# Kernel tuning notes

Measured on AMD Instinct MI355X. Metric: run time of the kernel, lower is better.

Reference implementation:

```python
import jax, jax.numpy as jnp
import numpy as np

B, S, D = 2, 2048, 768
H = 12
DK = D // H  # 64; dim_q = dim_k = dim_v
DFF = 3072
EPS = 1e-5


def layer_norm(x, w, b):
    mu = jnp.mean(x, axis=-1, keepdims=True)
    var = jnp.var(x, axis=-1, keepdims=True)
    return (x - mu) * jax.lax.rsqrt(var + EPS) * w + b


def setup_inputs() -> dict:
    key = jax.random.key(0)
    ks = jax.random.split(key, 12)
    s = 0.02
    return {
        "src": jax.random.normal(ks[0], (B, S, D), dtype=jnp.float32),
        # per-head projections stacked over heads: [H, D, DK]
        "Wq": jax.random.normal(ks[1], (H, D, DK), dtype=jnp.float32) * s,
        "bq": jnp.zeros((H, DK), dtype=jnp.float32),
        "Wk": jax.random.normal(ks[2], (H, D, DK), dtype=jnp.float32) * s,
        "bk": jnp.zeros((H, DK), dtype=jnp.float32),
        "Wv": jax.random.normal(ks[3], (H, D, DK), dtype=jnp.float32) * s,
        "bv": jnp.zeros((H, DK), dtype=jnp.float32),
        # output projection: [H*DK, D]
        "Wo": jax.random.normal(ks[4], (H * DK, D), dtype=jnp.float32) * s,
        "bo": jnp.zeros((D,), dtype=jnp.float32),
        "ln1_w": jnp.ones((D,), dtype=jnp.float32),
        "ln1_b": jnp.zeros((D,), dtype=jnp.float32),
        "W1": jax.random.normal(ks[5], (D, DFF), dtype=jnp.float32) * s,
        "b1": jnp.zeros((DFF,), dtype=jnp.float32),
        "W2": jax.random.normal(ks[6], (DFF, D), dtype=jnp.float32) * s,
        "b2": jnp.zeros((D,), dtype=jnp.float32),
        "ln2_w": jnp.ones((D,), dtype=jnp.float32),
        "ln2_b": jnp.zeros((D,), dtype=jnp.float32),
    }


def reference(src, Wq, bq, Wk, bk, Wv, bv, Wo, bo, ln1_w, ln1_b,
              W1, b1, W2, b2, ln2_w, ln2_b):
    # per-head q/k/v projections, batched over heads via einsum
    q = jnp.einsum('bsd,hdk->bhsk', src, Wq) + bq[None, :, None, :]
    k = jnp.einsum('bsd,hdk->bhsk', src, Wk) + bk[None, :, None, :]
    v = jnp.einsum('bsd,hdk->bhsk', src, Wv) + bv[None, :, None, :]
    scale = jnp.asarray(DK, src.dtype) ** 0.5
    scores = jnp.einsum('bhsk,bhtk->bhst', q, k) / scale  # [B,H,S,S]
    attn = jax.nn.softmax(scores, axis=-1)
    ctx = jnp.einsum('bhst,bhtk->bhsk', attn, v)
    # concat heads along feature dim (matches torch.cat over head outputs)
    ctx = ctx.transpose(0, 2, 1, 3).reshape(src.shape[0], src.shape[1], H * DK)
    attn_out = ctx @ Wo + bo
    x = layer_norm(src + attn_out, ln1_w, ln1_b)
    ff = jax.nn.relu(x @ W1 + b1) @ W2 + b2
    return layer_norm(x + ff, ln2_w, ln2_b)
```

## Files before the change

### kernel.cpp

```cpp
#include <hip/hip_runtime.h>
#include <hip/hip_bf16.h>

#define S_LEN 2048
#define DMODEL 768
#define NHEAD 12
#define DKH 64
#define DFF_K 3072
#define MROWS 4096
#define KSPLIT 2
#define KHALF (S_LEN / KSPLIT)

typedef __attribute__((ext_vector_type(8))) short bf16x8;
typedef __attribute__((ext_vector_type(8))) unsigned short us8;
typedef __attribute__((ext_vector_type(4))) float f32x4;

__device__ __forceinline__ float bfu2f(unsigned short u) {
  return __uint_as_float(((unsigned int)u) << 16);
}
__device__ __forceinline__ unsigned short f2bfu(float f) {
  __hip_bfloat16 h = __float2bfloat16(f);
  return *reinterpret_cast<unsigned short*>(&h);
}

__device__ __forceinline__ void async16(const unsigned short* g, unsigned short* l) {
  __builtin_amdgcn_global_load_lds(
      (const __attribute__((address_space(1))) unsigned int*)g,
      (__attribute__((address_space(3))) unsigned int*)l, 16, 0, 0);
}

__global__ __launch_bounds__(256) void convert_kernel(
    const float* __restrict__ in, unsigned short* __restrict__ out, int n4)
{
  const int i = blockIdx.x * 256 + threadIdx.x;
  if (i < n4) {
    float4 v = *(const float4*)(in + (size_t)i * 4);
    ushort4 o;
    o.x = f2bfu(v.x); o.y = f2bfu(v.y); o.z = f2bfu(v.z); o.w = f2bfu(v.w);
    *(ushort4*)(out + (size_t)i * 4) = o;
  }
}

__device__ __forceinline__ void transpose_conv_body(
    const float* in, unsigned short* out, int R, int Ctot, int head,
    int bx, int by, int tid)
{
  __shared__ float t[64][68];
  const int r0 = bx * 64;
  const int c0 = by * 64;
  const float* ib;
  int ld;
  if (head) { ib = in + (size_t)by * R * 64; ld = 64; }
  else      { ib = in + c0;                  ld = Ctot; }
  const int lr = tid >> 4;
  const int lc = (tid & 15) << 2;

#pragma unroll
  for (int rr = 0; rr < 4; ++rr) {
    const int row = rr * 16 + lr;
    float4 v = *(const float4*)(ib + (size_t)(r0 + row) * ld + lc);
    t[row][lc + 0] = v.x; t[row][lc + 1] = v.y;
    t[row][lc + 2] = v.z; t[row][lc + 3] = v.w;
  }
  __syncthreads();
#pragma unroll
  for (int rr = 0; rr < 4; ++rr) {
    const int oc = rr * 16 + lr;
    ushort4 o;
    o.x = f2bfu(t[lc + 0][oc]); o.y = f2bfu(t[lc + 1][oc]);
    o.z = f2bfu(t[lc + 2][oc]); o.w = f2bfu(t[lc + 3][oc]);
    *(ushort4*)(out + (size_t)(c0 + oc) * R + r0 + lc) = o;
  }
}

__global__ __launch_bounds__(256) void transpose_conv_kernel(
    const float* __restrict__ in, unsigned short* __restrict__ out,
    int R, int Ctot, int head)
{
  transpose_conv_body(in, out, R, Ctot, head, blockIdx.x, blockIdx.y, threadIdx.x);
}

__global__ __launch_bounds__(256) void transpose_conv4_kernel(
    const float* __restrict__ i0, const float* __restrict__ i1,
    const float* __restrict__ i2, const float* __restrict__ i3,
    unsigned short* __restrict__ o0, unsigned short* __restrict__ o1,
    unsigned short* __restrict__ o2, unsigned short* __restrict__ o3)
{
  const int z = blockIdx.z;
  const float* in = (z == 0) ? i0 : (z == 1) ? i1 : (z == 2) ? i2 : i3;
  unsigned short* out = (z == 0) ? o0 : (z == 1) ? o1 : (z == 2) ? o2 : o3;
  transpose_conv_body(in, out, DMODEL, DMODEL, (z < 3) ? 1 : 0,
                      blockIdx.x, blockIdx.y, threadIdx.x);
}

template<int BN>
__device__ __forceinline__ void stage_tile(
    const unsigned short* __restrict__ Ab,
    const unsigned short* __restrict__ Bb,
    unsigned short* As, unsigned short* Bs,
    int wid, int lane, int K, int kofs)
{
  const int r = lane >> 3;
  const int s = lane & 7;
#pragma unroll
  for (int p = 0; p < 4; ++p) {
    const int row = wid * 32 + p * 8 + r;
    async16(Ab + (size_t)row * K + kofs + ((s ^ (row & 7)) << 3),
            As + (size_t)(wid * 32 + p * 8) * 64);
  }
#pragma unroll
  for (int p = 0; p < BN / 32; ++p) {
    const int row = wid * (BN / 4) + p * 8 + r;
    async16(Bb + (size_t)row * K + kofs + ((s ^ (row & 7)) << 3),
            Bs + (size_t)(wid * (BN / 4) + p * 8) * 64);
  }
}

template<int BN>
__global__ __launch_bounds__(256) void mfma_gemm_kernel(
    const unsigned short* __restrict__ A,
    const unsigned short* __restrict__ BT,
    const float* __restrict__ bias,
    unsigned short* __restrict__ C,
    int K, int N, int relu, int klen, size_t out_stride)
{
  constexpr int WN = (BN == 128) ? 64 : 32;
  constexpr int NJ = WN / 16;
  __shared__ unsigned short As[2][128][64];
  __shared__ unsigned short Bs[2][BN][64];

  const int tid  = threadIdx.x;
  const int wid  = tid >> 6;
  const int lane = tid & 63;
  const int ml   = lane & 15;
  const int quad = lane >> 4;
  const int wm   = (wid & 1) * 64;
  const int wn   = (wid >> 1) * WN;
  const int row0 = blockIdx.x * 128;
  const int col0 = blockIdx.y * BN;
  const int zed  = blockIdx.z;
  const int kb0  = zed * klen;
  const int nsteps = klen >> 6;
  const int fsw = (ml & 7) << 4;

  const unsigned short* Ab = A  + (size_t)row0 * K + kb0;
  const unsigned short* Bb = BT + (size_t)col0 * K + kb0;

  f32x4 acc[4][NJ];
#pragma unroll
  for (int i = 0; i < 4; ++i)
#pragma unroll
    for (int j = 0; j < NJ; ++j)
#pragma unroll
      for (int r = 0; r < 4; ++r) acc[i][j][r] = 0.f;

  stage_tile<BN>(Ab, Bb, &As[0][0][0], &Bs[0][0][0], wid, lane, K, 0);
  __syncthreads();

  for (int st = 0; st < nsteps; ++st) {
    const int cur = st & 1;
    if (st + 1 < nsteps)
      stage_tile<BN>(Ab, Bb, &As[cur ^ 1][0][0], &Bs[cur ^ 1][0][0],
                     wid, lane, K, (st + 1) << 6);

    const char* Ac = (const char*)&As[cur][0][0];
    const char* Bc = (const char*)&Bs[cur][0][0];
#pragma unroll
    for (int h = 0; h < 2; ++h) {
      bf16x8 af[4], bfr[NJ];
#pragma unroll
      for (int i = 0; i < 4; ++i) {
        const int ar = wm + i * 16 + ml;
        af[i] = *(const bf16x8*)(Ac + ar * 128 + (((h << 6) + (quad << 4)) ^ fsw));
      }
#pragma unroll
      for (int j = 0; j < NJ; ++j) {
        const int br = wn + j * 16 + ml;
        bfr[j] = *(const bf16x8*)(Bc + br * 128 + (((h << 6) + (quad << 4)) ^ fsw));
      }
#pragma unroll
      for (int i = 0; i < 4; ++i)
#pragma unroll
        for (int j = 0; j < NJ; ++j)
          acc[i][j] = __builtin_amdgcn_mfma_f32_16x16x32_bf16(
              af[i], bfr[j], acc[i][j], 0, 0, 0);
    }
    __syncthreads();
  }

  unsigned short* Cz = C + (size_t)zed * out_stride;
#pragma unroll
  for (int j = 0; j < NJ; ++j) {
    const int col = col0 + wn + j * 16 + ml;
    const float bb = (zed == 0) ? bias[col] : 0.f;
#pragma unroll
    for (int i = 0; i < 4; ++i) {
      const int r0g = row0 + wm + i * 16 + (quad << 2);
#pragma unroll
      for (int r = 0; r < 4; ++r) {
        float v = acc[i][j][r] + bb;
        if (relu) v = fmaxf(v, 0.f);
        Cz[(size_t)(r0g + r) * N + col] = f2bfu(v);
      }
    }
  }
}

__global__ __launch_bounds__(256) void qkv_gemm_kernel(
    const unsigned short* __restrict__ A,
    const unsigned short* __restrict__ W0, const unsigned short* __restrict__ W1,
    const unsigned short* __restrict__ W2,
    const float* __restrict__ bq, const float* __restrict__ bk,
    const float* __restrict__ bv,
    unsigned short* __restrict__ C0, unsigned short* __restrict__ C1,
    unsigned short* __restrict__ C2)
{
  __shared__ unsigned short As[2][128][64];
  __shared__ unsigned short Bs[2][64][64];
  const int z = blockIdx.z;
  const unsigned short* BT = (z == 0) ? W0 : (z == 1) ? W1 : W2;
  const float* bias = (z == 0) ? bq : (z == 1) ? bk : bv;
  unsigned short* C = (z == 0) ? C0 : (z == 1) ? C1 : C2;
  const int K = DMODEL, N = DMODEL;

  const int tid  = threadIdx.x;
  const int wid  = tid >> 6;
  const int lane = tid & 63;
  const int ml   = lane & 15;
  const int quad = lane >> 4;
  const int wm   = (wid & 1) * 64;
  const int wn   = (wid >> 1) * 32;
  const int row0 = blockIdx.x * 128;
  const int col0 = blockIdx.y * 64;
  const int fsw = (ml & 7) << 4;

  const unsigned short* Ab = A  + (size_t)row0 * K;
  const unsigned short* Bb = BT + (size_t)col0 * K;

  f32x4 acc[4][2];
#pragma unroll
  for (int i = 0; i < 4; ++i)
#pragma unroll
    for (int j = 0; j < 2; ++j)
#pragma unroll
      for (int r = 0; r < 4; ++r) acc[i][j][r] = 0.f;

  stage_tile<64>(Ab, Bb, &As[0][0][0], &Bs[0][0][0], wid, lane, K, 0);
  __syncthreads();

  const int nsteps = K >> 6;
  for (int st = 0; st < nsteps; ++st) {
    const int cur = st & 1;
    if (st + 1 < nsteps)
      stage_tile<64>(Ab, Bb, &As[cur ^ 1][0][0], &Bs[cur ^ 1][0][0],
                     wid, lane, K, (st + 1) << 6);

    const char* Ac = (const char*)&As[cur][0][0];
    const char* Bc = (const char*)&Bs[cur][0][0];
#pragma unroll
    for (int h = 0; h < 2; ++h) {
      bf16x8 af[4], bfr[2];
#pragma unroll
      for (int i = 0; i < 4; ++i) {
        const int ar = wm + i * 16 + ml;
        af[i] = *(const bf16x8*)(Ac + ar * 128 + (((h << 6) + (quad << 4)) ^ fsw));
      }
#pragma unroll
      for (int j = 0; j < 2; ++j) {
        const int br = wn + j * 16 + ml;
        bfr[j] = *(const bf16x8*)(Bc + br * 128 + (((h << 6) + (quad << 4)) ^ fsw));
      }
#pragma unroll
      for (int i = 0; i < 4; ++i)
#pragma unroll
        for (int j = 0; j < 2; ++j)
          acc[i][j] = __builtin_amdgcn_mfma_f32_16x16x32_bf16(
              af[i], bfr[j], acc[i][j], 0, 0, 0);
    }
    __syncthreads();
  }

#pragma unroll
  for (int j = 0; j < 2; ++j) {
    const int col = col0 + wn + j * 16 + ml;
    const float bb = bias[col];
#pragma unroll
    for (int i = 0; i < 4; ++i) {
      const int r0g = row0 + wm + i * 16 + (quad << 2);
      if (z == 2) {
        const int bb_ = r0g >> 11, s = r0g & 2047;
        const int hh = col >> 6, dd = col & 63;
        ushort4 o;
        o.x = f2bfu(acc[i][j][0] + bb); o.y = f2bfu(acc[i][j][1] + bb);
        o.z = f2bfu(acc[i][j][2] + bb); o.w = f2bfu(acc[i][j][3] + bb);
        *(ushort4*)(C + ((size_t)((bb_ * NHEAD + hh) * DKH + dd)) * S_LEN + s) = o;
      } else {
#pragma unroll
        for (int r = 0; r < 4; ++r)
          C[(size_t)(r0g + r) * N + col] = f2bfu(acc[i][j][r] + bb);
      }
    }
  }
}

#define SCL2E 0.1803368822f
__global__ __launch_bounds__(256, 3) void flash_attn_mfma(
    const unsigned short* __restrict__ Q,
    const unsigned short* __restrict__ K,
    const unsigned short* __restrict__ VT,
    float* __restrict__ Opart,
    float* __restrict__ Lpart)
{
  __shared__ unsigned short Ks[64][64];
  __shared__ unsigned short Vs[64][64];
  __shared__ unsigned short QP[4][2][16][64];

  const int tid  = threadIdx.x;
  const int wid  = tid >> 6;
  const int lane = tid & 63;
  const int ml   = lane & 15;
  const int quad = lane >> 4;
  const int h    = blockIdx.x, b = blockIdx.y;
  const int q0   = (blockIdx.z >> 1) * 128;
  const int ks   = blockIdx.z & 1;
  const int kt0  = ks * KHALF;

  const size_t qkbase = ((size_t)b * S_LEN) * DMODEL + (size_t)h * DKH;
  const size_t vtbase = ((size_t)(b * NHEAD + h)) * DKH * S_LEN;

  const int sr  = tid >> 2;
  const int scb = (tid & 3) << 5;
  const int ssw = (sr & 7) << 4;
  const int fsw = (ml & 7) << 4;

  char* ksrow = (char*)&Ks[sr][0];
  char* vsrow = (char*)&Vs[sr][0];

  const int qrA = q0 + wid * 32 + ml;
  const int qrB = qrA + 16;
  const unsigned short* qpg = Q + qkbase;
  bf16x8 qfA0 = *(const bf16x8*)(qpg + (size_t)qrA * DMODEL + (quad << 3));
  bf16x8 qfA1 = *(const bf16x8*)(qpg + (size_t)qrA * DMODEL + 32 + (quad << 3));
  bf16x8 qfB0 = *(const bf16x8*)(qpg + (size_t)qrB * DMODEL + (quad << 3));
  bf16x8 qfB1 = *(const bf16x8*)(qpg + (size_t)qrB * DMODEL + 32 + (quad << 3));

  const unsigned short* pK = K + qkbase + (size_t)(kt0 + sr) * DMODEL + (scb >> 1);
  const unsigned short* pV = VT + vtbase + (size_t)sr * S_LEN + kt0 + (scb >> 1);

  float lsumA = 0.f, lsumB = 0.f;
  f32x4 oaccA[4], oaccB[4];
#pragma unroll
  for (int dt = 0; dt < 4; ++dt)
#pragma unroll
    for (int r = 0; r < 4; ++r) { oaccA[dt][r] = 0.f; oaccB[dt][r] = 0.f; }

  us8 rk0 = *(const us8*)(pK);
  us8 rk1 = *(const us8*)(pK + 8);
  us8 rv0 = *(const us8*)(pV);
  us8 rv1 = *(const us8*)(pV + 8);

  char* qpA = (char*)&QP[wid][0][ml][0];
  char* qpB = (char*)&QP[wid][1][ml][0];

  for (int kt = 0; kt < KHALF; kt += 64) {
    __syncthreads();
    *(us8*)(ksrow + ((scb +  0) ^ ssw)) = rk0;
    *(us8*)(ksrow + ((scb + 16) ^ ssw)) = rk1;
    *(us8*)(vsrow + ((scb +  0) ^ ssw)) = rv0;
    *(us8*)(vsrow + ((scb + 16) ^ ssw)) = rv1;
    __syncthreads();

    const int ktn = kt + 64;
    if (ktn < KHALF) {
      rk0 = *(const us8*)(pK + (size_t)ktn * DMODEL);
      rk1 = *(const us8*)(pK + (size_t)ktn * DMODEL + 8);
      rv0 = *(const us8*)(pV + ktn);
      rv1 = *(const us8*)(pV + ktn + 8);
    }

    f32x4 sA[4], sB[4];
#pragma unroll
    for (int mt = 0; mt < 4; ++mt)
#pragma unroll
      for (int r = 0; r < 4; ++r) { sA[mt][r] = 0.f; sB[mt][r] = 0.f; }
#pragma unroll
    for (int mt = 0; mt < 4; ++mt) {
      char* kr = (char*)&Ks[mt * 16 + ml][0];
      bf16x8 kf0 = *(const bf16x8*)(kr + (((quad << 4) +  0) ^ fsw));
      bf16x8 kf1 = *(const bf16x8*)(kr + (((quad << 4) + 64) ^ fsw));
      sA[mt] = __builtin_amdgcn_mfma_f32_16x16x32_bf16(kf0, qfA0, sA[mt], 0, 0, 0);
      sA[mt] = __builtin_amdgcn_mfma_f32_16x16x32_bf16(kf1, qfA1, sA[mt], 0, 0, 0);
      sB[mt] = __builtin_amdgcn_mfma_f32_16x16x32_bf16(kf0, qfB0, sB[mt], 0, 0, 0);
      sB[mt] = __builtin_amdgcn_mfma_f32_16x16x32_bf16(kf1, qfB1, sB[mt], 0, 0, 0);
    }

#pragma unroll
    for (int mt = 0; mt < 4; ++mt) {
      float e0 = exp2f(sA[mt][0] * SCL2E), e1 = exp2f(sA[mt][1] * SCL2E),
            e2 = exp2f(sA[mt][2] * SCL2E), e3 = exp2f(sA[mt][3] * SCL2E);
      lsumA += (e0 + e1) + (e2 + e3);
      ushort4 oA;
      oA.x = f2bfu(e0); oA.y = f2bfu(e1); oA.z = f2bfu(e2); oA.w = f2bfu(e3);
      *(ushort4*)(qpA + (((mt << 5) + (quad << 3)) ^ fsw)) = oA;
      e0 = exp2f(sB[mt][0] * SCL2E); e1 = exp2f(sB[mt][1] * SCL2E);
      e2 = exp2f(sB[mt][2] * SCL2E); e3 = exp2f(sB[mt][3] * SCL2E);
      lsumB += (e0 + e1) + (e2 + e3);
      ushort4 oB;
      oB.x = f2bfu(e0); oB.y = f2bfu(e1); oB.z = f2bfu(e2); oB.w = f2bfu(e3);
      *(ushort4*)(qpB + (((mt << 5) + (quad << 3)) ^ fsw)) = oB;
    }
    bf16x8 pfA0 = *(const bf16x8*)(qpA + (((quad << 4) +  0) ^ fsw));
    bf16x8 pfA1 = *(const bf16x8*)(qpA + (((quad << 4) + 64) ^ fsw));
    bf16x8 pfB0 = *(const bf16x8*)(qpB + (((quad << 4) +  0) ^ fsw));
    bf16x8 pfB1 = *(const bf16x8*)(qpB + (((quad << 4) + 64) ^ fsw));

#pragma unroll
    for (int dt = 0; dt < 4; ++dt) {
      char* vr = (char*)&Vs[dt * 16 + ml][0];
      bf16x8 vf0 = *(const bf16x8*)(vr + (((quad << 4) +  0) ^ fsw));
      bf16x8 vf1 = *(const bf16x8*)(vr + (((quad << 4) + 64) ^ fsw));
      oaccA[dt] = __builtin_amdgcn_mfma_f32_16x16x32_bf16(vf0, pfA0, oaccA[dt], 0, 0, 0);
      oaccA[dt] = __builtin_amdgcn_mfma_f32_16x16x32_bf16(vf1, pfA1, oaccA[dt], 0, 0, 0);
      oaccB[dt] = __builtin_amdgcn_mfma_f32_16x16x32_bf16(vf0, pfB0, oaccB[dt], 0, 0, 0);
      oaccB[dt] = __builtin_amdgcn_mfma_f32_16x16x32_bf16(vf1, pfB1, oaccB[dt], 0, 0, 0);
    }
  }

  lsumA += __shfl_xor(lsumA, 16);
  lsumA += __shfl_xor(lsumA, 32);
  lsumB += __shfl_xor(lsumB, 16);
  lsumB += __shfl_xor(lsumB, 32);
  const size_t lbase = (((size_t)(ks * 2 + b)) * NHEAD + h) * S_LEN;
  const size_t obaseA = (lbase + qrA) * DKH;
  const size_t obaseB = (lbase + qrB) * DKH;
#pragma unroll
  for (int dt = 0; dt < 4; ++dt) {
    *(f32x4*)&Opart[obaseA + dt * 16 + (quad << 2)] = oaccA[dt];
    *(f32x4*)&Opart[obaseB + dt * 16 + (quad << 2)] = oaccB[dt];
  }
  if (quad == 0) {
    Lpart[lbase + qrA] = lsumA;
    Lpart[lbase + qrB] = lsumB;
  }
}

__global__ __launch_bounds__(256) void attn_combine_kernel(
    const float* __restrict__ Op,
    const float* __restrict__ Lp,
    unsigned short* __restrict__ O)
{
  const int s = blockIdx.x & (S_LEN - 1);
  const int b = blockIdx.x >> 11;
  const int tid = threadIdx.x;
  const size_t ohalf = (size_t)2 * NHEAD * S_LEN * DKH;
  const size_t lhalf = (size_t)2 * NHEAD * S_LEN;
#pragma unroll
  for (int c = tid; c < DMODEL; c += 256) {
    const int hh = c >> 6, dd = c & 63;
    const size_t li = ((size_t)b * NHEAD + hh) * S_LEN + s;
    const size_t oi = li * DKH + dd;
    const float o = Op[oi] + Op[ohalf + oi];
    const float l = Lp[li] + Lp[lhalf + li];
    O[((size_t)b * S_LEN + s) * DMODEL + c] = f2bfu(o / l);
  }
}

__global__ __launch_bounds__(256) void add_ln_kernel(
    const void* __restrict__ X, const void* __restrict__ Y,
    const void* __restrict__ Y2,
    const float* __restrict__ w, const float* __restrict__ bvec,
    void* __restrict__ out, int xbf, int ybf, int obf)
{
  __shared__ float buf[DMODEL];
  __shared__ float rbuf[8];
  const int tid  = threadIdx.x;
  const int lane = tid & 63, wv = tid >> 6;
  const size_t base = (size_t)blockIdx.x * DMODEL;

  float s = 0.f, s2 = 0.f;
#pragma unroll
  for (int j = tid; j < DMODEL; j += 256) {
    float xv = xbf ? bfu2f(((const unsigned short*)X)[base + j])
                   : ((const float*)X)[base + j];
    float yv = ybf ? bfu2f(((const unsigned short*)Y)[base + j])
                   : ((const float*)Y)[base + j];
    float v = xv + yv;
    if (Y2) v += ybf ? bfu2f(((const unsigned short*)Y2)[base + j])
                     : ((const float*)Y2)[base + j];
    buf[j] = v; s += v; s2 += v * v;
  }
#pragma unroll
  for (int o = 32; o; o >>= 1) { s += __shfl_xor(s, o); s2 += __shfl_xor(s2, o); }
  if (lane == 0) { rbuf[wv] = s; rbuf[4 + wv] = s2; }
  __syncthreads();
  const float S  = rbuf[0] + rbuf[1] + rbuf[2] + rbuf[3];
  const float S2 = rbuf[4] + rbuf[5] + rbuf[6] + rbuf[7];
  const float mean = S * (1.f / (float)DMODEL);
  const float var  = S2 * (1.f / (float)DMODEL) - mean * mean;
  const float rstd = rsqrtf(var + 1e-5f);
#pragma unroll
  for (int j = tid; j < DMODEL; j += 256) {
    float v = (buf[j] - mean) * rstd * w[j] + bvec[j];
    if (obf) ((unsigned short*)out)[base + j] = f2bfu(v);
    else     ((float*)out)[base + j] = v;
  }
}

extern "C" void kernel_launch(void* const* d_in, const int* in_sizes, int n_in,
                              void* d_out, int out_size, void* d_ws, size_t ws_size,
                              hipStream_t stream) {
  const float* src  = (const float*)d_in[0];
  const float* Wq   = (const float*)d_in[1];
  const float* bq   = (const float*)d_in[2];
  const float* Wk   = (const float*)d_in[3];
  const float* bk   = (const float*)d_in[4];
  const float* Wv   = (const float*)d_in[5];
  const float* bv   = (const float*)d_in[6];
  const float* Wo   = (const float*)d_in[7];
  const float* bo   = (const float*)d_in[8];
  const float* ln1w = (const float*)d_in[9];
  const float* ln1b = (const float*)d_in[10];
  const float* W1   = (const float*)d_in[11];
  const float* b1   = (const float*)d_in[12];
  const float* W2   = (const float*)d_in[13];
  const float* b2   = (const float*)d_in[14];
  const float* ln2w = (const float*)d_in[15];
  const float* ln2b = (const float*)d_in[16];
  (void)ws_size; (void)in_sizes; (void)n_in; (void)out_size;

  unsigned short* p = (unsigned short*)d_ws;
  const size_t SEG = (size_t)MROWS * DMODEL;
  unsigned short* srcb = p; p += SEG;
  unsigned short* qb   = p; p += SEG;
  unsigned short* kb_  = p; p += SEG;
  unsigned short* vbT  = p; p += SEG;
  unsigned short* ctx  = p; p += SEG;
  unsigned short* ff   = p; p += (size_t)MROWS * DFF_K;
  unsigned short* wqt  = p; p += (size_t)DMODEL * DMODEL;
  unsigned short* wkt  = p; p += (size_t)DMODEL * DMODEL;
  unsigned short* wvt  = p; p += (size_t)DMODEL * DMODEL;
  unsigned short* wot  = p; p += (size_t)DMODEL * DMODEL;
  unsigned short* w1t  = p; p += (size_t)DMODEL * DFF_K;
  unsigned short* w2t  = p; p += (size_t)DMODEL * DFF_K;
  unsigned short* x1 = kb_;
  float* opart = (float*)ff;
  float* lpart = (float*)wqt;

  dim3 blk(256);

  convert_kernel<<<dim3(SEG / 1024), blk, 0, stream>>>(src, srcb, (int)(SEG / 4));
  transpose_conv4_kernel<<<dim3(12, 12, 4), blk, 0, stream>>>(
      Wq, Wk, Wv, Wo, wqt, wkt, wvt, wot);
  transpose_conv_kernel<<<dim3(12, 48), blk, 0, stream>>>(W1, w1t, DMODEL, DFF_K, 0);
  transpose_conv_kernel<<<dim3(48, 12), blk, 0, stream>>>(W2, w2t, DFF_K, DMODEL, 0);

  dim3 gqkv(MROWS / 128, DMODEL / 64, 3);
  qkv_gemm_kernel<<<gqkv, blk, 0, stream>>>(srcb, wqt, wkt, wvt, bq, bk, bv,
                                            qb, kb_, vbT);

  dim3 ga(NHEAD, 2, (S_LEN / 128) * KSPLIT);
  flash_attn_mfma<<<ga, blk, 0, stream>>>(qb, kb_, vbT, opart, lpart);
  attn_combine_kernel<<<dim3(MROWS), blk, 0, stream>>>(opart, lpart, ctx);

  dim3 gWo(MROWS / 128, DMODEL / 64, 2);
  mfma_gemm_kernel<64><<<gWo, blk, 0, stream>>>(ctx, wot, bo, qb,
                                                DMODEL, DMODEL, 0, DMODEL / 2, 2 * SEG);

  add_ln_kernel<<<dim3(MROWS), blk, 0, stream>>>(srcb, qb, vbT,
                                                 ln1w, ln1b, x1, 1, 1, 1);

  dim3 gF1(MROWS / 128, DFF_K / 128, 1);
  mfma_gemm_kernel<128><<<gF1, blk, 0, stream>>>(x1, w1t, b1, ff,
                                                 DMODEL, DFF_K, 1, DMODEL, 0);

  dim3 gW2(MROWS / 128, DMODEL / 64, 2);
  mfma_gemm_kernel<64><<<gW2, blk, 0, stream>>>(ff, w2t, b2, qb,
                                                DFF_K, DMODEL, 0, DFF_K / 2, 2 * SEG);

  add_ln_kernel<<<dim3(MROWS), blk, 0, stream>>>(x1, qb, vbT,
                                                 ln2w, ln2b, (float*)d_out, 1, 1, 0);
}
```

Baseline: 287.6 us.

## Load K/V attention fragments directly from global memory instead of LDS staging

New measurement: 334.6 us. 16.3% more time.

```diff
diff --git a/kernel.cpp b/kernel.cpp
--- a/kernel.cpp
+++ b/kernel.cpp
@@ -310,8 +310,6 @@
     float* __restrict__ Opart,
     float* __restrict__ Lpart)
 {
-  __shared__ unsigned short Ks[64][64];
-  __shared__ unsigned short Vs[64][64];
   __shared__ unsigned short QP[4][2][16][64];
 
   const int tid  = threadIdx.x;
@@ -327,13 +325,7 @@
   const size_t qkbase = ((size_t)b * S_LEN) * DMODEL + (size_t)h * DKH;
   const size_t vtbase = ((size_t)(b * NHEAD + h)) * DKH * S_LEN;
 
-  const int sr  = tid >> 2;
-  const int scb = (tid & 3) << 5;
-  const int ssw = (sr & 7) << 4;
   const int fsw = (ml & 7) << 4;
-
-  char* ksrow = (char*)&Ks[sr][0];
-  char* vsrow = (char*)&Vs[sr][0];
 
   const int qrA = q0 + wid * 32 + ml;
   const int qrB = qrA + 16;
@@ -343,8 +335,8 @@
   bf16x8 qfB0 = *(const bf16x8*)(qpg + (size_t)qrB * DMODEL + (quad << 3));
   bf16x8 qfB1 = *(const bf16x8*)(qpg + (size_t)qrB * DMODEL + 32 + (quad << 3));
 
-  const unsigned short* pK = K + qkbase + (size_t)(kt0 + sr) * DMODEL + (scb >> 1);
-  const unsigned short* pV = VT + vtbase + (size_t)sr * S_LEN + kt0 + (scb >> 1);
+  const unsigned short* Kf = K + qkbase + (size_t)(kt0 + ml) * DMODEL + (quad << 3);
+  const unsigned short* Vf = VT + vtbase + (size_t)ml * S_LEN + kt0 + (quad << 3);
 
   float lsumA = 0.f, lsumB = 0.f;
   f32x4 oaccA[4], oaccB[4];
@@ -353,30 +345,10 @@
 #pragma unroll
     for (int r = 0; r < 4; ++r) { oaccA[dt][r] = 0.f; oaccB[dt][r] = 0.f; }
 
-  us8 rk0 = *(const us8*)(pK);
-  us8 rk1 = *(const us8*)(pK + 8);
-  us8 rv0 = *(const us8*)(pV);
-  us8 rv1 = *(const us8*)(pV + 8);
-
   char* qpA = (char*)&QP[wid][0][ml][0];
   char* qpB = (char*)&QP[wid][1][ml][0];
 
   for (int kt = 0; kt < KHALF; kt += 64) {
-    __syncthreads();
-    *(us8*)(ksrow + ((scb +  0) ^ ssw)) = rk0;
-    *(us8*)(ksrow + ((scb + 16) ^ ssw)) = rk1;
-    *(us8*)(vsrow + ((scb +  0) ^ ssw)) = rv0;
-    *(us8*)(vsrow + ((scb + 16) ^ ssw)) = rv1;
-    __syncthreads();
-
-    const int ktn = kt + 64;
-    if (ktn < KHALF) {
-      rk0 = *(const us8*)(pK + (size_t)ktn * DMODEL);
-      rk1 = *(const us8*)(pK + (size_t)ktn * DMODEL + 8);
-      rv0 = *(const us8*)(pV + ktn);
-      rv1 = *(const us8*)(pV + ktn + 8);
-    }
-
     f32x4 sA[4], sB[4];
 #pragma unroll
     for (int mt = 0; mt < 4; ++mt)
@@ -384,13 +356,21 @@
       for (int r = 0; r < 4; ++r) { sA[mt][r] = 0.f; sB[mt][r] = 0.f; }
 #pragma unroll
     for (int mt = 0; mt < 4; ++mt) {
-      char* kr = (char*)&Ks[mt * 16 + ml][0];
-      bf16x8 kf0 = *(const bf16x8*)(kr + (((quad << 4) +  0) ^ fsw));
-      bf16x8 kf1 = *(const bf16x8*)(kr + (((quad << 4) + 64) ^ fsw));
+      const unsigned short* kr = Kf + (size_t)(kt + mt * 16) * DMODEL;
+      bf16x8 kf0 = *(const bf16x8*)(kr);
+      bf16x8 kf1 = *(const bf16x8*)(kr + 32);
       sA[mt] = __builtin_amdgcn_mfma_f32_16x16x32_bf16(kf0, qfA0, sA[mt], 0, 0, 0);
       sA[mt] = __builtin_amdgcn_mfma_f32_16x16x32_bf16(kf1, qfA1, sA[mt], 0, 0, 0);
       sB[mt] = __builtin_amdgcn_mfma_f32_16x16x32_bf16(kf0, qfB0, sB[mt], 0, 0, 0);
       sB[mt] = __builtin_amdgcn_mfma_f32_16x16x32_bf16(kf1, qfB1, sB[mt], 0, 0, 0);
+    }
+
+    bf16x8 vf[4][2];
+#pragma unroll
+    for (int dt = 0; dt < 4; ++dt) {
+      const unsigned short* vr = Vf + (size_t)(dt * 16) * S_LEN + kt;
+      vf[dt][0] = *(const bf16x8*)(vr);
+      vf[dt][1] = *(const bf16x8*)(vr + 32);
     }
 
 #pragma unroll
@@ -415,13 +395,10 @@
 
 #pragma unroll
     for (int dt = 0; dt < 4; ++dt) {
-      char* vr = (char*)&Vs[dt * 16 + ml][0];
-      bf16x8 vf0 = *(const bf16x8*)(vr + (((quad << 4) +  0) ^ fsw));
-      bf16x8 vf1 = *(const bf16x8*)(vr + (((quad << 4) + 64) ^ fsw));
-      oaccA[dt] = __builtin_amdgcn_mfma_f32_16x16x32_bf16(vf0, pfA0, oaccA[dt], 0, 0, 0);
-      oaccA[dt] = __builtin_amdgcn_mfma_f32_16x16x32_bf16(vf1, pfA1, oaccA[dt], 0, 0, 0);
-      oaccB[dt] = __builtin_amdgcn_mfma_f32_16x16x32_bf16(vf0, pfB0, oaccB[dt], 0, 0, 0);
-      oaccB[dt] = __builtin_amdgcn_mfma_f32_16x16x32_bf16(vf1, pfB1, oaccB[dt], 0, 0, 0);
+      oaccA[dt] = __builtin_amdgcn_mfma_f32_16x16x32_bf16(vf[dt][0], pfA0, oaccA[dt], 0, 0, 0);
+      oaccA[dt] = __builtin_amdgcn_mfma_f32_16x16x32_bf16(vf[dt][1], pfA1, oaccA[dt], 0, 0, 0);
+      oaccB[dt] = __builtin_amdgcn_mfma_f32_16x16x32_bf16(vf[dt][0], pfB0, oaccB[dt], 0, 0, 0);
+      oaccB[dt] = __builtin_amdgcn_mfma_f32_16x16x32_bf16(vf[dt][1], pfB1, oaccB[dt], 0, 0, 0);
     }
   }
 
```
